# Kernel tuning notes

Measured on AMD Instinct MI355X. Metric: run time of the kernel, lower is better.

## Reference

```python
import jax, jax.numpy as jnp
import numpy as np

INF = 1e20
NEG_FILL = -9e15  # value used by the torch module for masked entries
ALPHA = 0.2       # LeakyReLU negative slope
N, DIN, DOUT = 8192, 512, 512
EDGE_P = 0.1


def setup_inputs() -> dict:
    key = jax.random.key(0)
    k1, k2, k3, k4, k5 = jax.random.split(key, 5)
    inp = jax.random.normal(k1, (N, DIN), dtype=jnp.float32)
    # adjacency: 0.0 where an edge exists, -INF (non-edge) elsewhere
    u = jax.random.uniform(k2, (N, N), dtype=jnp.float32)
    adj = jnp.where(u < EDGE_P, 0.0, jnp.float32(-INF))
    # xavier_uniform with gain=1.414
    def xavier(k, shape, gain=1.414):
        fan_in, fan_out = shape[0], shape[1]
        bound = gain * np.sqrt(6.0 / (fan_in + fan_out))
        return jax.random.uniform(k, shape, dtype=jnp.float32, minval=-bound, maxval=bound)
    W = xavier(k3, (DIN, DOUT))
    a1 = xavier(k4, (DOUT, 1))
    a2 = xavier(k5, (DOUT, 1))
    return {"input": inp, "adj": adj, "W": W, "a1": a1, "a2": a2}


def reference(input, adj, W, a1, a2):
    h = input @ W                       # [N, DOUT]
    e1 = h @ a1                         # [N, 1] source score
    e2 = h @ a2                         # [N, 1] target score
    e = jax.nn.leaky_relu(e1 + e2.T, negative_slope=ALPHA)  # [N, N] additive score
    att = jnp.where(adj != -INF, e, jnp.float32(NEG_FILL))  # mask non-edges
    att = jax.nn.softmax(att, axis=-1)
    h_prime = att @ h                   # [N, DOUT]
    return jnp.tanh(h_prime)            # concat=True branch
```

## Files before the change

### kernel.cpp

```cpp
#include <hip/hip_runtime.h>
#include <stdint.h>

#define NN 8192
#define DD 512
#define SPLIT 4
#define ITERS_PER_SPLIT 16

typedef uint16_t u16;
typedef __bf16 bf16x8_t __attribute__((ext_vector_type(8)));
typedef float f32x4_t __attribute__((ext_vector_type(4)));
typedef uint32_t u32x4_t __attribute__((ext_vector_type(4)));

__device__ __forceinline__ u16 f2bf(float x) {
  uint32_t u = __builtin_bit_cast(uint32_t, x);
  u += 0x7FFFu + ((u >> 16) & 1u);
  return (u16)(u >> 16);
}
__device__ __forceinline__ float h2f(uint32_t bits) {
  return (float)__builtin_bit_cast(_Float16, (u16)bits);
}

__device__ __forceinline__ unsigned encf(float f) {
  unsigned u = __builtin_bit_cast(unsigned, f);
  return (u & 0x80000000u) ? ~u : (u | 0x80000000u);
}
__device__ __forceinline__ float decf(unsigned e) {
  unsigned u = (e & 0x80000000u) ? (e & 0x7FFFFFFFu) : ~e;
  return __builtin_bit_cast(float, u);
}

__global__ __launch_bounds__(256) void k_convert_W(const float* __restrict__ W,
                                                   u16* __restrict__ WT,
                                                   unsigned* __restrict__ maxenc) {
  int t = blockIdx.x * blockDim.x + threadIdx.x;
  if (t == 0) *maxenc = 0u;
  int n = t >> 6;
  int k8 = (t & 63) << 3;
  u16 tmp[8];
#pragma unroll
  for (int j = 0; j < 8; ++j) tmp[j] = f2bf(W[(size_t)(k8 + j) * DD + n]);
  uint32_t w0 = (uint32_t)tmp[0] | ((uint32_t)tmp[1] << 16);
  uint32_t w1 = (uint32_t)tmp[2] | ((uint32_t)tmp[3] << 16);
  uint32_t w2 = (uint32_t)tmp[4] | ((uint32_t)tmp[5] << 16);
  uint32_t w3 = (uint32_t)tmp[6] | ((uint32_t)tmp[7] << 16);
  *(uint4*)&WT[(size_t)n * DD + k8] = make_uint4(w0, w1, w2, w3);
}

__global__ __launch_bounds__(512) void k_gemm_h(const float* __restrict__ Af,
                                                const u16* __restrict__ BT,
                                                u16* __restrict__ HT,
                                                const float* __restrict__ a1,
                                                const float* __restrict__ a2,
                                                float* __restrict__ e1part,
                                                float* __restrict__ e2part) {
  __shared__ __align__(16) u16 As[64 * 32];
  __shared__ __align__(16) u16 Bs[128 * 32];
  const int tid = threadIdx.x;
  const int wid = tid >> 6, lane = tid & 63;
  const int wr = wid >> 1, wc = wid & 1;
  const int lr = lane & 15, kg = lane >> 4;
  const int rowBase = blockIdx.x * 64;
  const int colBase = blockIdx.y * 128;
  const int sr = tid >> 2, sc = tid & 3;
  f32x4_t acc[4] = {};
  for (int kt = 0; kt < 16; ++kt) {
    const int k0 = kt * 32 + sc * 8;
    if (tid < 256) {
      float4 f0 = *(const float4*)&Af[(size_t)(rowBase + sr) * DD + k0];
      float4 f1 = *(const float4*)&Af[(size_t)(rowBase + sr) * DD + k0 + 4];
      *(uint4*)&As[sr * 32 + sc * 8] = make_uint4(
          (uint32_t)f2bf(f0.x) | ((uint32_t)f2bf(f0.y) << 16),
          (uint32_t)f2bf(f0.z) | ((uint32_t)f2bf(f0.w) << 16),
          (uint32_t)f2bf(f1.x) | ((uint32_t)f2bf(f1.y) << 16),
          (uint32_t)f2bf(f1.z) | ((uint32_t)f2bf(f1.w) << 16));
    }
    *(uint4*)&Bs[sr * 32 + sc * 8] = *(const uint4*)&BT[(size_t)(colBase + sr) * DD + k0];
    __syncthreads();
    bf16x8_t af = *(const bf16x8_t*)&As[(wr * 16 + lr) * 32 + kg * 8];
    bf16x8_t bfv[4];
#pragma unroll
    for (int nt = 0; nt < 4; ++nt)
      bfv[nt] = *(const bf16x8_t*)&Bs[(wc * 64 + nt * 16 + lr) * 32 + kg * 8];
#pragma unroll
    for (int nt = 0; nt < 4; ++nt)
      acc[nt] = __builtin_amdgcn_mfma_f32_16x16x32_bf16(af, bfv[nt], acc[nt], 0, 0, 0);
    __syncthreads();
  }
  float a1v[4], a2v[4];
#pragma unroll
  for (int nt = 0; nt < 4; ++nt) {
    const int col = colBase + wc * 64 + nt * 16 + lr;
    a1v[nt] = a1[col];
    a2v[nt] = a2[col];
  }
  const int cg = blockIdx.y * 2 + wc;
  const int row0 = rowBase + wr * 16 + kg * 4;
#pragma unroll
  for (int nt = 0; nt < 4; ++nt) {
    const int col = colBase + wc * 64 + nt * 16 + lr;
    uint32_t lo = (uint32_t)f2bf(acc[nt][0]) | ((uint32_t)f2bf(acc[nt][1]) << 16);
    uint32_t hi = (uint32_t)f2bf(acc[nt][2]) | ((uint32_t)f2bf(acc[nt][3]) << 16);
    *(uint2*)&HT[(size_t)col * NN + row0] = make_uint2(lo, hi);
  }
#pragma unroll
  for (int r = 0; r < 4; ++r) {
    float t1 = 0.f, t2 = 0.f;
#pragma unroll
    for (int nt = 0; nt < 4; ++nt) {
      t1 += acc[nt][r] * a1v[nt];
      t2 += acc[nt][r] * a2v[nt];
    }
#pragma unroll
    for (int m = 1; m <= 8; m <<= 1) {
      t1 += __shfl_xor(t1, m);
      t2 += __shfl_xor(t2, m);
    }
    if (lr == 0) {
      e1part[(size_t)cg * NN + row0 + r] = t1;
      e2part[(size_t)cg * NN + row0 + r] = t2;
    }
  }
}

__global__ __launch_bounds__(256) void k_e12small(const float* __restrict__ e1part,
                                                  const float* __restrict__ e2part,
                                                  float* __restrict__ e1, float* __restrict__ e2,
                                                  unsigned* __restrict__ maxenc) {
  const int row = blockIdx.x * 256 + threadIdx.x;
  float s1 = 0.f, s2 = 0.f;
#pragma unroll
  for (int cg = 0; cg < 8; ++cg) {
    s1 += e1part[(size_t)cg * NN + row];
    s2 += e2part[(size_t)cg * NN + row];
  }
  e1[row] = s1;
  e2[row] = s2;
  atomicMax(maxenc, encf(s2));
}

__global__ __launch_bounds__(1024) void k_fused(const float* __restrict__ adj,
                                                const u16* __restrict__ HT,
                                                const float* __restrict__ e1,
                                                const float* __restrict__ e2,
                                                const unsigned* __restrict__ maxenc,
                                                u16* __restrict__ numpart,
                                                float* __restrict__ denpart) {
  __shared__ __align__(16) u16 P[2][128 * 128];
  __shared__ __align__(16) float e2s[256 * 12];
  __shared__ float partsum[2048];
  const int tid = threadIdx.x;
  const int wid = tid >> 6;
  const int lane = tid & 63;
  const int lr = lane & 15;
  const int kg = lane >> 4;
  const int b = blockIdx.x;
  const int xcd = b & 7;
  const int bz = xcd >> 1;
  const int rowBlock = (b >> 3) + ((xcd & 1) << 5);
  const int rowBase = rowBlock * 128;
  const int kk0 = bz * ITERS_PER_SPLIT;
  const int c = (tid >> 4) & 15;
  const int m = tid & 15;
  const int mt0 = tid >> 8;
  const int r0l = mt0 * 16 + m;
  const float e1r0 = e1[rowBase + r0l];
  const float e1r1 = e1[rowBase + r0l + 64];
  const float mE2 = decf(*maxenc);
  const float xb0 = e1r0 + mE2, xb1 = e1r1 + mE2;
  const float bnd0 = fmaxf(xb0, 0.2f * xb0);
  const float bnd1 = fmaxf(xb1, 0.2f * xb1);
  {
    const float* e2g = e2 + kk0 * 128;
    if (tid < 256) {
      float4 u0 = *(const float4*)(e2g + tid * 8);
      float4 u1 = *(const float4*)(e2g + tid * 8 + 4);
      *(float4*)&e2s[tid * 12] = u0;
      *(float4*)&e2s[tid * 12 + 4] = u1;
    }
  }
  const float* adjp0 = adj + (size_t)(rowBase + r0l) * NN + c * 8;
  const float* adjp1 = adjp0 + (size_t)64 * NN;
  const int n0 = wid * 32;
  const u16* btp0 = HT + (size_t)(n0 + 0 + lr) * NN + kg * 8;
  const u16* btp1 = HT + (size_t)(n0 + 16 + lr) * NN + kg * 8;
  float dsum0 = 0.f, dsum1 = 0.f;
  f32x4_t acc[8][2] = {};
  f32x4_t a00 = __builtin_nontemporal_load((const f32x4_t*)(adjp0 + kk0 * 128));
  f32x4_t a01 = __builtin_nontemporal_load((const f32x4_t*)(adjp0 + kk0 * 128 + 4));
  f32x4_t a10 = __builtin_nontemporal_load((const f32x4_t*)(adjp1 + kk0 * 128));
  f32x4_t a11 = __builtin_nontemporal_load((const f32x4_t*)(adjp1 + kk0 * 128 + 4));
  __syncthreads();
  for (int t = 0; t < ITERS_PER_SPLIT; ++t) {
    const int colBase = (kk0 + t) * 128;
    const float* eg = &e2s[(t * 16 + c) * 12];
    f32x4_t ev0 = *(const f32x4_t*)eg;
    f32x4_t ev1 = *(const f32x4_t*)(eg + 4);
    float ee[8] = {ev0[0], ev0[1], ev0[2], ev0[3], ev1[0], ev1[1], ev1[2], ev1[3]};
    float aa0[8] = {a00[0], a00[1], a00[2], a00[3], a01[0], a01[1], a01[2], a01[3]};
    float aa1[8] = {a10[0], a10[1], a10[2], a10[3], a11[0], a11[1], a11[2], a11[3]};
    float pv0[8], pv1[8];
#pragma unroll
    for (int j = 0; j < 8; ++j) {
      float x0 = e1r0 + ee[j];
      float s0 = fmaxf(x0, 0.2f * x0);
      float p0 = (aa0[j] > -1e19f) ? __expf(s0 - bnd0) : 0.f;
      pv0[j] = p0;
      dsum0 += p0;
      float x1 = e1r1 + ee[j];
      float s1 = fmaxf(x1, 0.2f * x1);
      float p1 = (aa1[j] > -1e19f) ? __expf(s1 - bnd1) : 0.f;
      pv1[j] = p1;
      dsum1 += p1;
    }
    {
      uint32_t w0 = (uint32_t)f2bf(pv0[0]) | ((uint32_t)f2bf(pv0[1]) << 16);
      uint32_t w1 = (uint32_t)f2bf(pv0[2]) | ((uint32_t)f2bf(pv0[3]) << 16);
      uint32_t w2 = (uint32_t)f2bf(pv0[4]) | ((uint32_t)f2bf(pv0[5]) << 16);
      uint32_t w3 = (uint32_t)f2bf(pv0[6]) | ((uint32_t)f2bf(pv0[7]) << 16);
      *(uint4*)&P[t & 1][tid * 8] = make_uint4(w0, w1, w2, w3);
      uint32_t v0 = (uint32_t)f2bf(pv1[0]) | ((uint32_t)f2bf(pv1[1]) << 16);
      uint32_t v1 = (uint32_t)f2bf(pv1[2]) | ((uint32_t)f2bf(pv1[3]) << 16);
      uint32_t v2 = (uint32_t)f2bf(pv1[4]) | ((uint32_t)f2bf(pv1[5]) << 16);
      uint32_t v3 = (uint32_t)f2bf(pv1[6]) | ((uint32_t)f2bf(pv1[7]) << 16);
      *(uint4*)&P[t & 1][(tid + 1024) * 8] = make_uint4(v0, v1, v2, v3);
    }
    if (t + 1 < ITERS_PER_SPLIT) {
      const float* q0 = adjp0 + colBase + 128;
      const float* q1 = adjp1 + colBase + 128;
      a00 = __builtin_nontemporal_load((const f32x4_t*)q0);
      a01 = __builtin_nontemporal_load((const f32x4_t*)(q0 + 4));
      a10 = __builtin_nontemporal_load((const f32x4_t*)q1);
      a11 = __builtin_nontemporal_load((const f32x4_t*)(q1 + 4));
    }
    bf16x8_t bc0 = *(const bf16x8_t*)(btp0 + colBase);
    bf16x8_t bc1 = *(const bf16x8_t*)(btp1 + colBase);
    asm volatile("s_waitcnt lgkmcnt(0)" ::: "memory");
    __builtin_amdgcn_s_barrier();
    const u16* pb = &P[t & 1][0];
#pragma unroll
    for (int ks = 0; ks < 4; ++ks) {
      bf16x8_t bn0, bn1;
      if (ks < 3) {
        const int co = colBase + (ks + 1) * 32;
        bn0 = *(const bf16x8_t*)(btp0 + co);
        bn1 = *(const bf16x8_t*)(btp1 + co);
      }
#pragma unroll
      for (int mt = 0; mt < 8; ++mt) {
        bf16x8_t af = *(const bf16x8_t*)(pb + mt * 2048 + ks * 512 + lane * 8);
        acc[mt][0] = __builtin_amdgcn_mfma_f32_16x16x32_bf16(af, bc0, acc[mt][0], 0, 0, 0);
        acc[mt][1] = __builtin_amdgcn_mfma_f32_16x16x32_bf16(af, bc1, acc[mt][1], 0, 0, 0);
      }
      if (ks < 3) { bc0 = bn0; bc1 = bn1; }
    }
  }
  partsum[tid] = dsum0;
  partsum[tid + 1024] = dsum1;
  __syncthreads();
  if (tid < 128) {
    const int rr = tid;
    const int rlo = rr & 63;
    const int off = (rr >> 6) << 10;
    float s = 0.f;
#pragma unroll
    for (int cc = 0; cc < 16; ++cc)
      s += partsum[off + (rlo >> 4) * 256 + cc * 16 + (rlo & 15)];
    denpart[(size_t)bz * NN + rowBase + rr] = s;
  }
  u16* np = numpart + (size_t)bz * NN * DD;
#pragma unroll
  for (int mt = 0; mt < 8; ++mt)
#pragma unroll
    for (int nt = 0; nt < 2; ++nt)
#pragma unroll
      for (int r = 0; r < 4; ++r) {
        const int rowL = mt * 16 + kg * 4 + r;
        _Float16 hv = (_Float16)acc[mt][nt][r];
        __builtin_nontemporal_store(__builtin_bit_cast(u16, hv),
                                    &np[(size_t)(rowBase + rowL) * DD + n0 + nt * 16 + lr]);
      }
}

__global__ __launch_bounds__(256) void k_combine(const u16* __restrict__ num,
                                                 const float* __restrict__ den,
                                                 float* __restrict__ out) {
  const size_t idx = (size_t)blockIdx.x * 256 + threadIdx.x;
  const int row = (int)(idx >> 6);
  float d = den[row] + den[NN + row] + den[2 * NN + row] + den[3 * NN + row];
  const u32x4_t* nv = (const u32x4_t*)num;
  const size_t stride = (size_t)NN * DD / 8;
  float s[8] = {};
#pragma unroll
  for (int sl = 0; sl < 4; ++sl) {
    u32x4_t q = __builtin_nontemporal_load(nv + sl * stride + idx);
    s[0] += h2f(q[0] & 0xffff); s[1] += h2f(q[0] >> 16);
    s[2] += h2f(q[1] & 0xffff); s[3] += h2f(q[1] >> 16);
    s[4] += h2f(q[2] & 0xffff); s[5] += h2f(q[2] >> 16);
    s[6] += h2f(q[3] & 0xffff); s[7] += h2f(q[3] >> 16);
  }
  const float inv = (d > 0.f) ? 1.f / d : 0.f;
  f32x4_t o0, o1;
#pragma unroll
  for (int j = 0; j < 4; ++j) o0[j] = 1.f - 2.f / (__expf(2.f * (s[j] * inv)) + 1.f);
#pragma unroll
  for (int j = 0; j < 4; ++j) o1[j] = 1.f - 2.f / (__expf(2.f * (s[4 + j] * inv)) + 1.f);
  __builtin_nontemporal_store(o0, ((f32x4_t*)out) + idx * 2);
  __builtin_nontemporal_store(o1, ((f32x4_t*)out) + idx * 2 + 1);
}

extern "C" void kernel_launch(void* const* d_in, const int* in_sizes, int n_in,
                              void* d_out, int out_size, void* d_ws, size_t ws_size,
                              hipStream_t stream) {
  const float* input = (const float*)d_in[0];
  const float* adj   = (const float*)d_in[1];
  const float* W     = (const float*)d_in[2];
  const float* a1    = (const float*)d_in[3];
  const float* a2    = (const float*)d_in[4];
  float* out = (float*)d_out;
  char* ws = (char*)d_ws;

  u16* hT        = (u16*)ws;
  float* e1      = (float*)(ws + 8388608);
  float* e2      = (float*)(ws + 8421376);
  unsigned* mx   = (unsigned*)(ws + 8454144);
  float* denp    = (float*)(ws + 8454400);
  float* e1p     = (float*)(ws + 8585472);
  float* e2p     = (float*)(ws + 8847616);
  u16* nump      = (u16*)(ws + 9109760);
  u16* WT        = (u16*)(ws + 9109760);

  hipLaunchKernelGGL(k_convert_W, dim3(128), dim3(256), 0, stream, W, WT, mx);
  hipLaunchKernelGGL(k_gemm_h, dim3(128, 4), dim3(512), 0, stream, input, WT, hT, a1, a2, e1p, e2p);
  hipLaunchKernelGGL(k_e12small, dim3(32), dim3(256), 0, stream, e1p, e2p, e1, e2, mx);
  hipLaunchKernelGGL(k_fused, dim3(64 * SPLIT), dim3(1024), 0, stream, adj, hT, e1, e2, mx, nump, denp);
  hipLaunchKernelGGL(k_combine, dim3(2048), dim3(256), 0, stream, nump, denp, out);
}
```

Baseline: 175.9 us.

## Warp-specialize fused attention kernel into producer and MFMA consumer halves

Splits each 1024-thread block into two halves. Threads 512-1023 build the masked exp probability tile from adj into double-buffered shared memory one iteration ahead, and threads 0-511 run the MFMA P·H accumulation on the previous tile. Row tiles shrink from 128 to 64 rows, so the grid doubles, and each MMA wave now covers 64 output columns instead of 32. This is meant to overlap the adjacency streaming and exp work with the tensor-core GEMM. The cost is that HT is re-read from memory twice as often, because each block now covers half as many rows, and the two halves rely on carefully matched barrier counts.

Result: slower. 221.9 us (+26.2%).

```diff
diff --git a/kernel.cpp b/kernel.cpp
--- a/kernel.cpp
+++ b/kernel.cpp
@@ -145,30 +145,19 @@
                                                 const unsigned* __restrict__ maxenc,
                                                 u16* __restrict__ numpart,
                                                 float* __restrict__ denpart) {
-  __shared__ __align__(16) u16 P[2][128 * 128];
+  __shared__ __align__(16) u16 P[2][64 * 128];
   __shared__ __align__(16) float e2s[256 * 12];
-  __shared__ float partsum[2048];
+  __shared__ float partsum[1024];
   const int tid = threadIdx.x;
-  const int wid = tid >> 6;
   const int lane = tid & 63;
   const int lr = lane & 15;
   const int kg = lane >> 4;
   const int b = blockIdx.x;
   const int xcd = b & 7;
   const int bz = xcd >> 1;
-  const int rowBlock = (b >> 3) + ((xcd & 1) << 5);
-  const int rowBase = rowBlock * 128;
+  const int rowBlock = (b >> 3) + ((xcd & 1) << 6);
+  const int rowBase = rowBlock * 64;
   const int kk0 = bz * ITERS_PER_SPLIT;
-  const int c = (tid >> 4) & 15;
-  const int m = tid & 15;
-  const int mt0 = tid >> 8;
-  const int r0l = mt0 * 16 + m;
-  const float e1r0 = e1[rowBase + r0l];
-  const float e1r1 = e1[rowBase + r0l + 64];
-  const float mE2 = decf(*maxenc);
-  const float xb0 = e1r0 + mE2, xb1 = e1r1 + mE2;
-  const float bnd0 = fmaxf(xb0, 0.2f * xb0);
-  const float bnd1 = fmaxf(xb1, 0.2f * xb1);
   {
     const float* e2g = e2 + kk0 * 128;
     if (tid < 256) {
@@ -178,107 +167,166 @@
       *(float4*)&e2s[tid * 12 + 4] = u1;
     }
   }
-  const float* adjp0 = adj + (size_t)(rowBase + r0l) * NN + c * 8;
-  const float* adjp1 = adjp0 + (size_t)64 * NN;
-  const int n0 = wid * 32;
-  const u16* btp0 = HT + (size_t)(n0 + 0 + lr) * NN + kg * 8;
-  const u16* btp1 = HT + (size_t)(n0 + 16 + lr) * NN + kg * 8;
-  float dsum0 = 0.f, dsum1 = 0.f;
-  f32x4_t acc[8][2] = {};
-  f32x4_t a00 = __builtin_nontemporal_load((const f32x4_t*)(adjp0 + kk0 * 128));
-  f32x4_t a01 = __builtin_nontemporal_load((const f32x4_t*)(adjp0 + kk0 * 128 + 4));
-  f32x4_t a10 = __builtin_nontemporal_load((const f32x4_t*)(adjp1 + kk0 * 128));
-  f32x4_t a11 = __builtin_nontemporal_load((const f32x4_t*)(adjp1 + kk0 * 128 + 4));
-  __syncthreads();
-  for (int t = 0; t < ITERS_PER_SPLIT; ++t) {
-    const int colBase = (kk0 + t) * 128;
-    const float* eg = &e2s[(t * 16 + c) * 12];
-    f32x4_t ev0 = *(const f32x4_t*)eg;
-    f32x4_t ev1 = *(const f32x4_t*)(eg + 4);
-    float ee[8] = {ev0[0], ev0[1], ev0[2], ev0[3], ev1[0], ev1[1], ev1[2], ev1[3]};
-    float aa0[8] = {a00[0], a00[1], a00[2], a00[3], a01[0], a01[1], a01[2], a01[3]};
-    float aa1[8] = {a10[0], a10[1], a10[2], a10[3], a11[0], a11[1], a11[2], a11[3]};
-    float pv0[8], pv1[8];
-#pragma unroll
-    for (int j = 0; j < 8; ++j) {
-      float x0 = e1r0 + ee[j];
-      float s0 = fmaxf(x0, 0.2f * x0);
-      float p0 = (aa0[j] > -1e19f) ? __expf(s0 - bnd0) : 0.f;
-      pv0[j] = p0;
-      dsum0 += p0;
-      float x1 = e1r1 + ee[j];
-      float s1 = fmaxf(x1, 0.2f * x1);
-      float p1 = (aa1[j] > -1e19f) ? __expf(s1 - bnd1) : 0.f;
-      pv1[j] = p1;
-      dsum1 += p1;
-    }
+
+  if (tid < 512) {
+    const int wid = tid >> 6;
+    const int n0 = wid * 64;
+    const u16* btp0 = HT + (size_t)(n0 + 0 + lr) * NN + kg * 8;
+    const u16* btp1 = HT + (size_t)(n0 + 16 + lr) * NN + kg * 8;
+    const u16* btp2 = HT + (size_t)(n0 + 32 + lr) * NN + kg * 8;
+    const u16* btp3 = HT + (size_t)(n0 + 48 + lr) * NN + kg * 8;
+    f32x4_t acc[4][4] = {};
+    __syncthreads();
+    bf16x8_t bc0 = *(const bf16x8_t*)(btp0 + kk0 * 128);
+    bf16x8_t bc1 = *(const bf16x8_t*)(btp1 + kk0 * 128);
+    bf16x8_t bc2 = *(const bf16x8_t*)(btp2 + kk0 * 128);
+    bf16x8_t bc3 = *(const bf16x8_t*)(btp3 + kk0 * 128);
+    asm volatile("s_waitcnt lgkmcnt(0)" ::: "memory");
+    __builtin_amdgcn_s_barrier();
+#pragma unroll 1
+    for (int t = 0; t < ITERS_PER_SPLIT; ++t) {
+      const int colBase = (kk0 + t) * 128;
+      const u16* pb = &P[t & 1][0];
+#pragma unroll
+      for (int ks = 0; ks < 4; ++ks) {
+        bf16x8_t bn0, bn1, bn2, bn3;
+        if (ks < 3) {
+          const int co = colBase + (ks + 1) * 32;
+          bn0 = *(const bf16x8_t*)(btp0 + co);
+          bn1 = *(const bf16x8_t*)(btp1 + co);
+          bn2 = *(const bf16x8_t*)(btp2 + co);
+          bn3 = *(const bf16x8_t*)(btp3 + co);
+        }
+#pragma unroll
+        for (int mt = 0; mt < 4; ++mt) {
+          bf16x8_t af = *(const bf16x8_t*)(pb + mt * 2048 + ks * 512 + lane * 8);
+          acc[mt][0] = __builtin_amdgcn_mfma_f32_16x16x32_bf16(af, bc0, acc[mt][0], 0, 0, 0);
+          acc[mt][1] = __builtin_amdgcn_mfma_f32_16x16x32_bf16(af, bc1, acc[mt][1], 0, 0, 0);
+          acc[mt][2] = __builtin_amdgcn_mfma_f32_16x16x32_bf16(af, bc2, acc[mt][2], 0, 0, 0);
+          acc[mt][3] = __builtin_amdgcn_mfma_f32_16x16x32_bf16(af, bc3, acc[mt][3], 0, 0, 0);
+        }
+        if (ks < 3) { bc0 = bn0; bc1 = bn1; bc2 = bn2; bc3 = bn3; }
+      }
+      if (t + 1 < ITERS_PER_SPLIT) {
+        const int co = colBase + 128;
+        bc0 = *(const bf16x8_t*)(btp0 + co);
+        bc1 = *(const bf16x8_t*)(btp1 + co);
+        bc2 = *(const bf16x8_t*)(btp2 + co);
+        bc3 = *(const bf16x8_t*)(btp3 + co);
+      }
+      asm volatile("s_waitcnt lgkmcnt(0)" ::: "memory");
+      __builtin_amdgcn_s_barrier();
+    }
+    u16* np = numpart + (size_t)bz * NN * DD;
+#pragma unroll
+    for (int mt = 0; mt < 4; ++mt)
+#pragma unroll
+      for (int nt = 0; nt < 4; ++nt)
+#pragma unroll
+        for (int r = 0; r < 4; ++r) {
+          const int rowL = mt * 16 + kg * 4 + r;
+          _Float16 hv = (_Float16)acc[mt][nt][r];
+          __builtin_nontemporal_store(__builtin_bit_cast(u16, hv),
+                                      &np[(size_t)(rowBase + rowL) * DD + n0 + nt * 16 + lr]);
+        }
+    __syncthreads();
+  } else {
+    const int pt = tid - 512;
+    const int c = (pt >> 4) & 15;
+    const int m = pt & 15;
+    const int mt0 = pt >> 8;
+    const int r0l = mt0 * 16 + m;
+    const float e1r0 = e1[rowBase + r0l];
+    const float e1r1 = e1[rowBase + r0l + 32];
+    const float mE2 = decf(*maxenc);
+    const float xb0 = e1r0 + mE2, xb1 = e1r1 + mE2;
+    const float bnd0 = fmaxf(xb0, 0.2f * xb0);
+    const float bnd1 = fmaxf(xb1, 0.2f * xb1);
+    const float* adjp0 = adj + (size_t)(rowBase + r0l) * NN + c * 8;
+    const float* adjp1 = adjp0 + (size_t)32 * NN;
+    float dsum0 = 0.f, dsum1 = 0.f;
+    f32x4_t a00 = __builtin_nontemporal_load((const f32x4_t*)(adjp0 + kk0 * 128));
+    f32x4_t a01 = __builtin_nontemporal_load((const f32x4_t*)(adjp0 + kk0 * 128 + 4));
+    f32x4_t a10 = __builtin_nontemporal_load((const f32x4_t*)(adjp1 + kk0 * 128));
+    f32x4_t a11 = __builtin_nontemporal_load((const f32x4_t*)(adjp1 + kk0 * 128 + 4));
+    __syncthreads();
+
+#define BUILD(tt, qb)                                                                         \
+    {                                                                                         \
+      const float* eg_ = &e2s[((tt) * 16 + c) * 12];                                          \
+      f32x4_t ev0_ = *(const f32x4_t*)eg_;                                                    \
+      f32x4_t ev1_ = *(const f32x4_t*)(eg_ + 4);                                              \
+      float ee_[8] = {ev0_[0], ev0_[1], ev0_[2], ev0_[3], ev1_[0], ev1_[1], ev1_[2], ev1_[3]};\
+      float aa0_[8] = {a00[0], a00[1], a00[2], a00[3], a01[0], a01[1], a01[2], a01[3]};       \
+      float aa1_[8] = {a10[0], a10[1], a10[2], a10[3], a11[0], a11[1], a11[2], a11[3]};       \
+      float pv0_[8], pv1_[8];                                                                 \
+      _Pragma("unroll")                                                                       \
+      for (int j = 0; j < 8; ++j) {                                                           \
+        float x0_ = e1r0 + ee_[j];                                                            \
+        float s0_ = fmaxf(x0_, 0.2f * x0_);                                                   \
+        float p0_ = (aa0_[j] > -1e19f) ? __expf(s0_ - bnd0) : 0.f;                            \
+        pv0_[j] = p0_; dsum0 += p0_;                                                          \
+        float x1_ = e1r1 + ee_[j];                                                            \
+        float s1_ = fmaxf(x1_, 0.2f * x1_);                                                   \
+        float p1_ = (aa1_[j] > -1e19f) ? __expf(s1_ - bnd1) : 0.f;                            \
+        pv1_[j] = p1_; dsum1 += p1_;                                                          \
+      }                                                                                       \
+      uint32_t w0_ = (uint32_t)f2bf(pv0_[0]) | ((uint32_t)f2bf(pv0_[1]) << 16);               \
+      uint32_t w1_ = (uint32_t)f2bf(pv0_[2]) | ((uint32_t)f2bf(pv0_[3]) << 16);               \
+      uint32_t w2_ = (uint32_t)f2bf(pv0_[4]) | ((uint32_t)f2bf(pv0_[5]) << 16);               \
+      uint32_t w3_ = (uint32_t)f2bf(pv0_[6]) | ((uint32_t)f2bf(pv0_[7]) << 16);               \
+      *(uint4*)&(qb)[pt * 8] = make_uint4(w0_, w1_, w2_, w3_);                                \
+      uint32_t v0_ = (uint32_t)f2bf(pv1_[0]) | ((uint32_t)f2bf(pv1_[1]) << 16);               \
+      uint32_t v1_ = (uint32_t)f2bf(pv1_[2]) | ((uint32_t)f2bf(pv1_[3]) << 16);               \
+      uint32_t v2_ = (uint32_t)f2bf(pv1_[4]) | ((uint32_t)f2bf(pv1_[5]) << 16);               \
+      uint32_t v3_ = (uint32_t)f2bf(pv1_[6]) | ((uint32_t)f2bf(pv1_[7]) << 16);               \
+      *(uint4*)&(qb)[(pt + 512) * 8] = make_uint4(v0_, v1_, v2_, v3_);                        \
+    }
+
+    BUILD(0, (&P[0][0]))
     {
-      uint32_t w0 = (uint32_t)f2bf(pv0[0]) | ((uint32_t)f2bf(pv0[1]) << 16);
-      uint32_t w1 = (uint32_t)f2bf(pv0[2]) | ((uint32_t)f2bf(pv0[3]) << 16);
-      uint32_t w2 = (uint32_t)f2bf(pv0[4]) | ((uint32_t)f2bf(pv0[5]) << 16);
-      uint32_t w3 = (uint32_t)f2bf(pv0[6]) | ((uint32_t)f2bf(pv0[7]) << 16);
-      *(uint4*)&P[t & 1][tid * 8] = make_uint4(w0, w1, w2, w3);
-      uint32_t v0 = (uint32_t)f2bf(pv1[0]) | ((uint32_t)f2bf(pv1[1]) << 16);
-      uint32_t v1 = (uint32_t)f2bf(pv1[2]) | ((uint32_t)f2bf(pv1[3]) << 16);
-      uint32_t v2 = (uint32_t)f2bf(pv1[4]) | ((uint32_t)f2bf(pv1[5]) << 16);
-      uint32_t v3 = (uint32_t)f2bf(pv1[6]) | ((uint32_t)f2bf(pv1[7]) << 16);
-      *(uint4*)&P[t & 1][(tid + 1024) * 8] = make_uint4(v0, v1, v2, v3);
-    }
-    if (t + 1 < ITERS_PER_SPLIT) {
-      const float* q0 = adjp0 + colBase + 128;
-      const float* q1 = adjp1 + colBase + 128;
+      const float* q0 = adjp0 + (kk0 + 1) * 128;
+      const float* q1 = adjp1 + (kk0 + 1) * 128;
       a00 = __builtin_nontemporal_load((const f32x4_t*)q0);
       a01 = __builtin_nontemporal_load((const f32x4_t*)(q0 + 4));
       a10 = __builtin_nontemporal_load((const f32x4_t*)q1);
       a11 = __builtin_nontemporal_load((const f32x4_t*)(q1 + 4));
     }
-    bf16x8_t bc0 = *(const bf16x8_t*)(btp0 + colBase);
-    bf16x8_t bc1 = *(const bf16x8_t*)(btp1 + colBase);
     asm volatile("s_waitcnt lgkmcnt(0)" ::: "memory");
     __builtin_amdgcn_s_barrier();
-    const u16* pb = &P[t & 1][0];
-#pragma unroll
-    for (int ks = 0; ks < 4; ++ks) {
-      bf16x8_t bn0, bn1;
-      if (ks < 3) {
-        const int co = colBase + (ks + 1) * 32;
-        bn0 = *(const bf16x8_t*)(btp0 + co);
-        bn1 = *(const bf16x8_t*)(btp1 + co);
+#pragma unroll 1
+    for (int t = 0; t < ITERS_PER_SPLIT; ++t) {
+      if (t + 1 < ITERS_PER_SPLIT) {
+        u16* qb = &P[(t + 1) & 1][0];
+        BUILD(t + 1, qb)
+        if (t + 2 < ITERS_PER_SPLIT) {
+          const float* q0 = adjp0 + (size_t)(kk0 + t + 2) * 128;
+          const float* q1 = adjp1 + (size_t)(kk0 + t + 2) * 128;
+          a00 = __builtin_nontemporal_load((const f32x4_t*)q0);
+          a01 = __builtin_nontemporal_load((const f32x4_t*)(q0 + 4));
+          a10 = __builtin_nontemporal_load((const f32x4_t*)q1);
+          a11 = __builtin_nontemporal_load((const f32x4_t*)(q1 + 4));
+        }
       }
-#pragma unroll
-      for (int mt = 0; mt < 8; ++mt) {
-        bf16x8_t af = *(const bf16x8_t*)(pb + mt * 2048 + ks * 512 + lane * 8);
-        acc[mt][0] = __builtin_amdgcn_mfma_f32_16x16x32_bf16(af, bc0, acc[mt][0], 0, 0, 0);
-        acc[mt][1] = __builtin_amdgcn_mfma_f32_16x16x32_bf16(af, bc1, acc[mt][1], 0, 0, 0);
-      }
-      if (ks < 3) { bc0 = bn0; bc1 = bn1; }
-    }
-  }
-  partsum[tid] = dsum0;
-  partsum[tid + 1024] = dsum1;
-  __syncthreads();
-  if (tid < 128) {
-    const int rr = tid;
-    const int rlo = rr & 63;
-    const int off = (rr >> 6) << 10;
-    float s = 0.f;
-#pragma unroll
-    for (int cc = 0; cc < 16; ++cc)
-      s += partsum[off + (rlo >> 4) * 256 + cc * 16 + (rlo & 15)];
-    denpart[(size_t)bz * NN + rowBase + rr] = s;
-  }
-  u16* np = numpart + (size_t)bz * NN * DD;
-#pragma unroll
-  for (int mt = 0; mt < 8; ++mt)
-#pragma unroll
-    for (int nt = 0; nt < 2; ++nt)
-#pragma unroll
-      for (int r = 0; r < 4; ++r) {
-        const int rowL = mt * 16 + kg * 4 + r;
-        _Float16 hv = (_Float16)acc[mt][nt][r];
-        __builtin_nontemporal_store(__builtin_bit_cast(u16, hv),
-                                    &np[(size_t)(rowBase + rowL) * DD + n0 + nt * 16 + lr]);
-      }
+      asm volatile("s_waitcnt lgkmcnt(0)" ::: "memory");
+      __builtin_amdgcn_s_barrier();
+    }
+#undef BUILD
+    partsum[pt] = dsum0;
+    partsum[pt + 512] = dsum1;
+    __syncthreads();
+    if (pt < 64) {
+      const int rr = pt;
+      const int off = (rr >= 32) ? 512 : 0;
+      const int mt_ = (rr & 31) >> 4;
+      const int m_ = rr & 15;
+      float s = 0.f;
+#pragma unroll
+      for (int cc = 0; cc < 16; ++cc)
+        s += partsum[off + mt_ * 256 + cc * 16 + m_];
+      denpart[(size_t)bz * NN + rowBase + rr] = s;
+    }
+  }
 }
 
 __global__ __launch_bounds__(256) void k_combine(const u16* __restrict__ num,
@@ -332,6 +380,6 @@
   hipLaunchKernelGGL(k_convert_W, dim3(128), dim3(256), 0, stream, W, WT, mx);
   hipLaunchKernelGGL(k_gemm_h, dim3(128, 4), dim3(512), 0, stream, input, WT, hT, a1, a2, e1p, e2p);
   hipLaunchKernelGGL(k_e12small, dim3(32), dim3(256), 0, stream, e1p, e2p, e1, e2, mx);
-  hipLaunchKernelGGL(k_fused, dim3(64 * SPLIT), dim3(1024), 0, stream, adj, hT, e1, e2, mx, nump, denp);
+  hipLaunchKernelGGL(k_fused, dim3(128 * SPLIT), dim3(1024), 0, stream, adj, hT, e1, e2, mx, nump, denp);
   hipLaunchKernelGGL(k_combine, dim3(2048), dim3(256), 0, stream, nump, denp, out);
 }
```
